# Kernel optimization log

Measured on AMD Instinct MI355X. Metric: run time of the kernel, lower is better.

Reference implementation:

```python
import jax, jax.numpy as jnp
import numpy as np

C, D, H, W = 48, 128, 128, 128
N = 2097152


def setup_inputs() -> dict:
    key = jax.random.key(0)
    k1, k2, k3 = jax.random.split(key, 3)
    # normalized coords in [-1, 1] as expected by grid_sample(align_corners=True)
    ray_pts = jax.random.uniform(k1, (N, 3), jnp.float32) * 2.0 - 1.0
    k0 = jax.random.normal(k2, (1, C, D, H, W), jnp.float32) * 1e-4
    former_k0_cur = jax.random.normal(k3, (1, C, D, H, W), jnp.float32)
    return {"ray_pts": ray_pts, "k0": k0, "former_k0_cur": former_k0_cur}


def _grid_sample_trilinear(grid, pts):
    # grid: [C, D, H, W]; pts: [N, 3] with (x, y, z) in [-1, 1] mapping to (W, H, D)
    c, d, h, w = grid.shape
    x, y, z = pts[:, 0], pts[:, 1], pts[:, 2]
    # align_corners=True: -1 -> 0, +1 -> size-1
    ix = (x + 1.0) * 0.5 * (w - 1)
    iy = (y + 1.0) * 0.5 * (h - 1)
    iz = (z + 1.0) * 0.5 * (d - 1)
    x0f, y0f, z0f = jnp.floor(ix), jnp.floor(iy), jnp.floor(iz)
    wx, wy, wz = ix - x0f, iy - y0f, iz - z0f
    x0 = jnp.clip(x0f.astype(jnp.int32), 0, w - 1)
    x1 = jnp.clip(x0f.astype(jnp.int32) + 1, 0, w - 1)
    y0 = jnp.clip(y0f.astype(jnp.int32), 0, h - 1)
    y1 = jnp.clip(y0f.astype(jnp.int32) + 1, 0, h - 1)
    z0 = jnp.clip(z0f.astype(jnp.int32), 0, d - 1)
    z1 = jnp.clip(z0f.astype(jnp.int32) + 1, 0, d - 1)

    def g(zi, yi, xi):
        return grid[:, zi, yi, xi]  # [C, N] gather

    out = (
        g(z0, y0, x0) * ((1 - wx) * (1 - wy) * (1 - wz))
        + g(z0, y0, x1) * (wx * (1 - wy) * (1 - wz))
        + g(z0, y1, x0) * ((1 - wx) * wy * (1 - wz))
        + g(z0, y1, x1) * (wx * wy * (1 - wz))
        + g(z1, y0, x0) * ((1 - wx) * (1 - wy) * wz)
        + g(z1, y0, x1) * (wx * (1 - wy) * wz)
        + g(z1, y1, x0) * ((1 - wx) * wy * wz)
        + g(z1, y1, x1) * (wx * wy * wz)
    )
    return out  # [C, N]


def reference(ray_pts, k0, former_k0_cur):
    # faithful to torch: full dense grid add, then trilinear grid_sample lookup
    grid = (former_k0_cur + k0)[0]  # [C, D, H, W]
    feats = _grid_sample_trilinear(grid, ray_pts)  # [C, N]
    return feats.T  # [N, C]
```

## Files before the change

### kernel.cpp

```cpp
#include <hip/hip_runtime.h>
#include <hip/hip_bf16.h>
#include <cstdint>

#define CCH 48
#define DD 128
#define HH 128
#define WW 128
#define NVOX (DD*HH*WW)
#define NPTS 2097152

typedef unsigned int uint;
typedef unsigned short ushort_t;

__device__ __forceinline__ ushort_t f2bf_rne(float f) {
    uint u = __float_as_uint(f);
    uint r = (u + 0x7fffu + ((u >> 16) & 1u)) >> 16;
    return (ushort_t)r;
}

__global__ __launch_bounds__(256) void fuse_transpose_kernel(
    const float* __restrict__ k0, const float* __restrict__ former,
    ushort_t* __restrict__ grid_t)
{
    const int v = blockIdx.x * 256 + threadIdx.x;
    float vals[CCH];
#pragma unroll
    for (int c = 0; c < CCH; ++c)
        vals[c] = k0[(size_t)c * NVOX + v] + former[(size_t)c * NVOX + v];

    uint4* dst = reinterpret_cast<uint4*>(grid_t + (size_t)v * CCH);
#pragma unroll
    for (int i = 0; i < 6; ++i) {
        uint4 u;
        u.x = (uint)f2bf_rne(vals[i*8+0]) | ((uint)f2bf_rne(vals[i*8+1]) << 16);
        u.y = (uint)f2bf_rne(vals[i*8+2]) | ((uint)f2bf_rne(vals[i*8+3]) << 16);
        u.z = (uint)f2bf_rne(vals[i*8+4]) | ((uint)f2bf_rne(vals[i*8+5]) << 16);
        u.w = (uint)f2bf_rne(vals[i*8+6]) | ((uint)f2bf_rne(vals[i*8+7]) << 16);
        dst[i] = u;
    }
}

__device__ __forceinline__ void corner_acc(const ushort_t* __restrict__ base,
                                           float wgt, float acc[24])
{
    const uint4* p = reinterpret_cast<const uint4*>(base);
    uint4 a = p[0], b = p[1], c = p[2];
    uint us[12] = {a.x,a.y,a.z,a.w, b.x,b.y,b.z,b.w, c.x,c.y,c.z,c.w};
#pragma unroll
    for (int j = 0; j < 12; ++j) {
        acc[2*j]   = fmaf(wgt, __uint_as_float(us[j] << 16),        acc[2*j]);
        acc[2*j+1] = fmaf(wgt, __uint_as_float(us[j] & 0xffff0000u), acc[2*j+1]);
    }
}

__global__ __launch_bounds__(256) void sample_kernel(
    const float* __restrict__ pts, const ushort_t* __restrict__ grid_t,
    float* __restrict__ out)
{
    const int tid = blockIdx.x * 256 + threadIdx.x;
    const int n   = tid >> 1;
    const int sub = tid & 1;

    const float px = pts[n*3+0], py = pts[n*3+1], pz = pts[n*3+2];
    const float ix = (px + 1.0f) * 63.5f;
    const float iy = (py + 1.0f) * 63.5f;
    const float iz = (pz + 1.0f) * 63.5f;
    const float xf = floorf(ix), yf = floorf(iy), zf = floorf(iz);
    const float wx = ix - xf, wy = iy - yf, wz = iz - zf;
    int x0 = (int)xf, y0 = (int)yf, z0 = (int)zf;
    int x1 = x0 + 1, y1 = y0 + 1, z1 = z0 + 1;
    x0 = min(max(x0,0), WW-1); x1 = min(max(x1,0), WW-1);
    y0 = min(max(y0,0), HH-1); y1 = min(max(y1,0), HH-1);
    z0 = min(max(z0,0), DD-1); z1 = min(max(z1,0), DD-1);

    const float wx0 = 1.0f - wx, wy0 = 1.0f - wy, wz0 = 1.0f - wz;

    float acc[24];
#pragma unroll
    for (int k = 0; k < 24; ++k) acc[k] = 0.0f;

    const int HWn = HH*WW;
    const int bz0 = z0*HWn, bz1 = z1*HWn;
    const int by0 = y0*WW,  by1 = y1*WW;
    const int so  = sub*24;

    corner_acc(grid_t + (size_t)(bz0+by0+x0)*CCH + so, wx0*wy0*wz0, acc);
    corner_acc(grid_t + (size_t)(bz0+by0+x1)*CCH + so, wx *wy0*wz0, acc);
    corner_acc(grid_t + (size_t)(bz0+by1+x0)*CCH + so, wx0*wy *wz0, acc);
    corner_acc(grid_t + (size_t)(bz0+by1+x1)*CCH + so, wx *wy *wz0, acc);
    corner_acc(grid_t + (size_t)(bz1+by0+x0)*CCH + so, wx0*wy0*wz , acc);
    corner_acc(grid_t + (size_t)(bz1+by0+x1)*CCH + so, wx *wy0*wz , acc);
    corner_acc(grid_t + (size_t)(bz1+by1+x0)*CCH + so, wx0*wy *wz , acc);
    corner_acc(grid_t + (size_t)(bz1+by1+x1)*CCH + so, wx *wy *wz , acc);

    float4* o = reinterpret_cast<float4*>(out + (size_t)n*CCH + so);
#pragma unroll
    for (int i = 0; i < 6; ++i)
        o[i] = make_float4(acc[i*4+0], acc[i*4+1], acc[i*4+2], acc[i*4+3]);
}

__global__ __launch_bounds__(256) void sample_naive(
    const float* __restrict__ pts, const float* __restrict__ k0,
    const float* __restrict__ former, float* __restrict__ out)
{
    const int n = blockIdx.x * 256 + threadIdx.x;
    if (n >= NPTS) return;
    const float px = pts[n*3+0], py = pts[n*3+1], pz = pts[n*3+2];
    const float ix = (px + 1.0f) * 63.5f;
    const float iy = (py + 1.0f) * 63.5f;
    const float iz = (pz + 1.0f) * 63.5f;
    const float xf = floorf(ix), yf = floorf(iy), zf = floorf(iz);
    const float wx = ix - xf, wy = iy - yf, wz = iz - zf;
    int x0 = (int)xf, y0 = (int)yf, z0 = (int)zf;
    int x1 = x0 + 1, y1 = y0 + 1, z1 = z0 + 1;
    x0 = min(max(x0,0), WW-1); x1 = min(max(x1,0), WW-1);
    y0 = min(max(y0,0), HH-1); y1 = min(max(y1,0), HH-1);
    z0 = min(max(z0,0), DD-1); z1 = min(max(z1,0), DD-1);
    const float wx0 = 1.0f - wx, wy0 = 1.0f - wy, wz0 = 1.0f - wz;
    const int HWn = HH*WW;
    const int v000 = z0*HWn + y0*WW + x0, v100 = z0*HWn + y0*WW + x1;
    const int v010 = z0*HWn + y1*WW + x0, v110 = z0*HWn + y1*WW + x1;
    const int v001 = z1*HWn + y0*WW + x0, v101 = z1*HWn + y0*WW + x1;
    const int v011 = z1*HWn + y1*WW + x0, v111 = z1*HWn + y1*WW + x1;
    const float w000 = wx0*wy0*wz0, w100 = wx*wy0*wz0;
    const float w010 = wx0*wy*wz0,  w110 = wx*wy*wz0;
    const float w001 = wx0*wy0*wz,  w101 = wx*wy0*wz;
    const float w011 = wx0*wy*wz,   w111 = wx*wy*wz;
    for (int c = 0; c < CCH; ++c) {
        const float* g0 = k0     + (size_t)c * NVOX;
        const float* g1 = former + (size_t)c * NVOX;
        float s = 0.0f;
        s += w000 * (g0[v000] + g1[v000]);
        s += w100 * (g0[v100] + g1[v100]);
        s += w010 * (g0[v010] + g1[v010]);
        s += w110 * (g0[v110] + g1[v110]);
        s += w001 * (g0[v001] + g1[v001]);
        s += w101 * (g0[v101] + g1[v101]);
        s += w011 * (g0[v011] + g1[v011]);
        s += w111 * (g0[v111] + g1[v111]);
        out[(size_t)n*CCH + c] = s;
    }
}

extern "C" void kernel_launch(void* const* d_in, const int* in_sizes, int n_in,
                              void* d_out, int out_size, void* d_ws, size_t ws_size,
                              hipStream_t stream) {
    const float* ray_pts = (const float*)d_in[0];
    const float* k0      = (const float*)d_in[1];
    const float* former  = (const float*)d_in[2];
    float* out = (float*)d_out;

    const size_t need = (size_t)NVOX * CCH * sizeof(ushort_t);
    if (ws_size >= need) {
        ushort_t* grid_t = (ushort_t*)d_ws;
        fuse_transpose_kernel<<<NVOX/256, 256, 0, stream>>>(k0, former, grid_t);
        sample_kernel<<<(NPTS*2)/256, 256, 0, stream>>>(ray_pts, grid_t, out);
    } else {
        sample_naive<<<NPTS/256, 256, 0, stream>>>(ray_pts, k0, former, out);
    }
}
```

Baseline: 646.2 us.

## Interleave per-thread channel chunks and issue all corner loads upfront

Changes the split of the 48 channels between the two threads of a point: instead of contiguous halves, each thread takes alternating 16-byte chunks, so the pair's loads for one corner sit next to each other. All 8 corners' 24 uint4 loads are issued before any FMA to raise memory-level parallelism, and launch bounds request 4 blocks per CU. Output stores are interleaved the same way. Holding 24 uint4 registers live raises register pressure, which may conflict with the occupancy hint.

Result: slower. 1.229 ms (+90.2%).

```diff
diff --git a/kernel.cpp b/kernel.cpp
--- a/kernel.cpp
+++ b/kernel.cpp
@@ -40,20 +40,7 @@
     }
 }
 
-__device__ __forceinline__ void corner_acc(const ushort_t* __restrict__ base,
-                                           float wgt, float acc[24])
-{
-    const uint4* p = reinterpret_cast<const uint4*>(base);
-    uint4 a = p[0], b = p[1], c = p[2];
-    uint us[12] = {a.x,a.y,a.z,a.w, b.x,b.y,b.z,b.w, c.x,c.y,c.z,c.w};
-#pragma unroll
-    for (int j = 0; j < 12; ++j) {
-        acc[2*j]   = fmaf(wgt, __uint_as_float(us[j] << 16),        acc[2*j]);
-        acc[2*j+1] = fmaf(wgt, __uint_as_float(us[j] & 0xffff0000u), acc[2*j+1]);
-    }
-}
-
-__global__ __launch_bounds__(256) void sample_kernel(
+__global__ __launch_bounds__(256, 4) void sample_kernel(
     const float* __restrict__ pts, const ushort_t* __restrict__ grid_t,
     float* __restrict__ out)
 {
@@ -72,31 +59,72 @@
     x0 = min(max(x0,0), WW-1); x1 = min(max(x1,0), WW-1);
     y0 = min(max(y0,0), HH-1); y1 = min(max(y1,0), HH-1);
     z0 = min(max(z0,0), DD-1); z1 = min(max(z1,0), DD-1);
-
     const float wx0 = 1.0f - wx, wy0 = 1.0f - wy, wz0 = 1.0f - wz;
-
-    float acc[24];
-#pragma unroll
-    for (int k = 0; k < 24; ++k) acc[k] = 0.0f;
 
     const int HWn = HH*WW;
     const int bz0 = z0*HWn, bz1 = z1*HWn;
     const int by0 = y0*WW,  by1 = y1*WW;
-    const int so  = sub*24;
 
-    corner_acc(grid_t + (size_t)(bz0+by0+x0)*CCH + so, wx0*wy0*wz0, acc);
-    corner_acc(grid_t + (size_t)(bz0+by0+x1)*CCH + so, wx *wy0*wz0, acc);
-    corner_acc(grid_t + (size_t)(bz0+by1+x0)*CCH + so, wx0*wy *wz0, acc);
-    corner_acc(grid_t + (size_t)(bz0+by1+x1)*CCH + so, wx *wy *wz0, acc);
-    corner_acc(grid_t + (size_t)(bz1+by0+x0)*CCH + so, wx0*wy0*wz , acc);
-    corner_acc(grid_t + (size_t)(bz1+by0+x1)*CCH + so, wx *wy0*wz , acc);
-    corner_acc(grid_t + (size_t)(bz1+by1+x0)*CCH + so, wx0*wy *wz , acc);
-    corner_acc(grid_t + (size_t)(bz1+by1+x1)*CCH + so, wx *wy *wz , acc);
+    const int vox[8] = { bz0+by0+x0, bz0+by0+x1, bz0+by1+x0, bz0+by1+x1,
+                         bz1+by0+x0, bz1+by0+x1, bz1+by1+x0, bz1+by1+x1 };
+    const float w[8] = { wx0*wy0*wz0, wx*wy0*wz0, wx0*wy*wz0, wx*wy*wz0,
+                         wx0*wy0*wz , wx*wy0*wz , wx0*wy*wz , wx*wy*wz  };
 
-    float4* o = reinterpret_cast<float4*>(out + (size_t)n*CCH + so);
+    float acc[3][8];
 #pragma unroll
-    for (int i = 0; i < 6; ++i)
-        o[i] = make_float4(acc[i*4+0], acc[i*4+1], acc[i*4+2], acc[i*4+3]);
+    for (int j = 0; j < 3; ++j)
+#pragma unroll
+        for (int q = 0; q < 8; ++q) acc[j][q] = 0.0f;
+
+    uint4 LA[4][3];
+#pragma unroll
+    for (int c = 0; c < 4; ++c) {
+        const uint4* p = reinterpret_cast<const uint4*>(grid_t + (size_t)vox[c] * CCH);
+#pragma unroll
+        for (int j = 0; j < 3; ++j) LA[c][j] = p[2*j + sub];
+    }
+    uint4 LB[4][3];
+#pragma unroll
+    for (int c = 0; c < 4; ++c) {
+        const uint4* p = reinterpret_cast<const uint4*>(grid_t + (size_t)vox[4+c] * CCH);
+#pragma unroll
+        for (int j = 0; j < 3; ++j) LB[c][j] = p[2*j + sub];
+    }
+
+#pragma unroll
+    for (int c = 0; c < 4; ++c) {
+        const float wc = w[c];
+#pragma unroll
+        for (int j = 0; j < 3; ++j) {
+            const uint* us = reinterpret_cast<const uint*>(&LA[c][j]);
+#pragma unroll
+            for (int q = 0; q < 4; ++q) {
+                acc[j][2*q]   = fmaf(wc, __uint_as_float(us[q] << 16),         acc[j][2*q]);
+                acc[j][2*q+1] = fmaf(wc, __uint_as_float(us[q] & 0xffff0000u), acc[j][2*q+1]);
+            }
+        }
+    }
+#pragma unroll
+    for (int c = 0; c < 4; ++c) {
+        const float wc = w[4+c];
+#pragma unroll
+        for (int j = 0; j < 3; ++j) {
+            const uint* us = reinterpret_cast<const uint*>(&LB[c][j]);
+#pragma unroll
+            for (int q = 0; q < 4; ++q) {
+                acc[j][2*q]   = fmaf(wc, __uint_as_float(us[q] << 16),         acc[j][2*q]);
+                acc[j][2*q+1] = fmaf(wc, __uint_as_float(us[q] & 0xffff0000u), acc[j][2*q+1]);
+            }
+        }
+    }
+
+    float4* o = reinterpret_cast<float4*>(out + (size_t)n * CCH);
+#pragma unroll
+    for (int j = 0; j < 3; ++j) {
+        const int g = 2*j + sub;
+        o[2*g+0] = make_float4(acc[j][0], acc[j][1], acc[j][2], acc[j][3]);
+        o[2*g+1] = make_float4(acc[j][4], acc[j][5], acc[j][6], acc[j][7]);
+    }
 }
 
 __global__ __launch_bounds__(256) void sample_naive(
```
